# Kernel optimization log

Hardware: AMD Instinct MI355X
Metric: run time of the kernel (lower is better)

Reference implementation:

```python
import jax, jax.numpy as jnp
import numpy as np

jax.config.update("jax_enable_x64", True)  # Q16.16 int64 fixed-point arithmetic requires 64-bit ints

F = 16                 # FixedPointConfig.COMPUTE_FRAC_BITS (Q16.16)
ONE = 1 << F

B, S, D_IN, D_OUT = 2, 2048, 4096, 4096


def setup_inputs() -> dict:
    key = jax.random.key(0)
    k1, k2 = jax.random.split(key)
    x = jax.random.normal(k1, (B, S, D_IN), dtype=jnp.float32)
    weight = jax.random.normal(k2, (D_OUT, D_IN), dtype=jnp.float32)
    return {"x": x, "weight": weight}


def _to_fixed(x):
    # to_fixed_point: float -> Q16.16 int64
    return jnp.round(x * ONE).astype(jnp.int64)


def _activation_quant_fixed(xf):
    # per-token 8-bit quant/dequant, all in Q16.16 integer arithmetic
    max_vals = jnp.max(jnp.abs(xf), axis=-1, keepdims=True)
    min_val = int(1e-5 * ONE)  # == 0 at frac_bits=16 (faithful to source)
    max_vals = jnp.maximum(max_vals, min_val)
    target_max = 127 << F
    # fixed_div(target_max, max_vals, F, F, F): (a << F) // b
    scale = (target_max << F) // max_vals
    # fixed_mul(x, scale, F, F, F): (a*b) >> F  (arithmetic shift == floor-div)
    x_scaled = (xf * scale) >> F
    x_clamped = jnp.clip(x_scaled, -(128 << F), 127 << F)
    # fixed_reciprocal(scale, F, F): (1 << 2F) // scale
    scale_inv = (1 << (2 * F)) // scale
    return (x_clamped * scale_inv) >> F


def reference(x, weight):
    # --- quantize_weights() ---
    wf = _to_fixed(weight)                                   # Q16.16
    mean_abs = jnp.sum(jnp.abs(wf)) // wf.size               # fixed_mean (Q16.16 scalar)
    # fixed_div(wf, mean_abs, F, F, 0) -> integer-valued; round+clamp to {-1,0,1}
    w_ternary = jnp.clip(wf // mean_abs, -1, 1).astype(jnp.int8)

    # --- forward ---
    xq = _activation_quant_fixed(_to_fixed(x))               # [B,S,D] Q16.16 int64
    xq2 = xq.reshape(-1, D_IN)
    # Ternary GEMM replacing the per-output-feature masked-sum loop.
    # |xq| <= 128<<16 ~ 8.4e6 and K=4096 => |acc| <= 3.4e10 < 2^53, so a
    acc = jnp.dot(xq2.astype(jnp.float64), w_ternary.astype(jnp.float64).T)
    out = jnp.round(acc).astype(jnp.int64)
    out = out.astype(jnp.int32).astype(jnp.int64)            # replicate torch .to(int32) wrap
    scale_inv = (1 << (2 * F)) // mean_abs                   # fixed_reciprocal of weight_scale
    out = (out * scale_inv) >> F                             # fixed_mul dequant/rescale
    out = out.reshape(B, S, D_OUT)
    return out.astype(jnp.float32) / ONE                     # from_fixed_point
```

## Files before the change

### kernel.cpp

```cpp
#include <hip/hip_runtime.h>
#include <stdint.h>

typedef int v4i  __attribute__((ext_vector_type(4)));
typedef int v16i __attribute__((ext_vector_type(16)));

static constexpr int Mdim = 4096;
static constexpr int Ndim = 4096;
static constexpr int Kdim = 4096;

static constexpr size_t TILE_BYTES  = 128u * 4096u;
static constexpr size_t OFF_BT      = 1u << 20;
static constexpr size_t OFF_A0      = 17u << 20;
static constexpr size_t PLANE_BYTES = 16u << 20;

__device__ __forceinline__ void gload16(const void* g, void* l) {
  __builtin_amdgcn_global_load_lds(
      (const __attribute__((address_space(1))) char*)g,
      (__attribute__((address_space(3))) char*)l, 16, 0, 0);
}

__global__ void k_wsum(const float* __restrict__ w, unsigned long long* __restrict__ ws) {
  int tid = blockIdx.x * blockDim.x + threadIdx.x;
  int stride = gridDim.x * blockDim.x;
  const float4* w4 = (const float4*)w;
  const int n4 = (Ndim * Kdim) / 4;
  unsigned long long s = 0;
  for (int i = tid; i < n4; i += stride) {
    float4 v = w4[i];
    int a = (int)rintf(v.x * 65536.f);
    int b = (int)rintf(v.y * 65536.f);
    int c = (int)rintf(v.z * 65536.f);
    int d = (int)rintf(v.w * 65536.f);
    unsigned u = (unsigned)(a < 0 ? -a : a) + (unsigned)(b < 0 ? -b : b)
               + (unsigned)(c < 0 ? -c : c) + (unsigned)(d < 0 ? -d : d);
    s += u;
  }
  #pragma unroll
  for (int off = 32; off > 0; off >>= 1) s += __shfl_down(s, off, 64);
  if ((threadIdx.x & 63) == 0) atomicAdd(ws, s);
}

__global__ void k_scalars(unsigned long long* ws) {
  unsigned long long s = ws[0];
  long long mean_abs = (long long)(s >> 24);
  if (mean_abs < 1) mean_abs = 1;
  long long siw = (long long)((1ULL << 32) / (unsigned long long)mean_abs);
  ((long long*)ws)[1] = siw;
  ((long long*)ws)[2] = mean_abs;
}

__global__ void k_tern(const float* __restrict__ w, const long long* __restrict__ scal,
                       int8_t* __restrict__ bt) {
  int t = blockIdx.x * 256 + threadIdx.x;
  int mean_abs = (int)scal[2];
  int nt = t >> 15;
  int kc = (t >> 7) & 255;
  int r  = t & 127;
  int row = nt * 128 + r;
  const float4* src = (const float4*)(w + (size_t)row * Kdim + kc * 16);
  int words[4];
  #pragma unroll
  for (int j = 0; j < 4; ++j) {
    float4 v = src[j];
    float e[4] = {v.x, v.y, v.z, v.w};
    int wrd = 0;
    #pragma unroll
    for (int q = 0; q < 4; ++q) {
      int f = (int)rintf(e[q] * 65536.f);
      int tv = (f >= mean_abs ? 1 : 0) - (f < 0 ? 1 : 0);
      wrd |= (tv & 0xff) << (8 * q);
    }
    words[j] = wrd;
  }
  *(int4*)(bt + (size_t)nt * TILE_BYTES + (size_t)kc * 2048 + (size_t)r * 16) =
      make_int4(words[0], words[1], words[2], words[3]);
}

__global__ void k_actq2(const float* __restrict__ x,
                        int8_t* __restrict__ a0, int8_t* __restrict__ a1, int8_t* __restrict__ a2) {
  int m   = blockIdx.x;
  int tid = threadIdx.x;
  const float4* src = (const float4*)(x + (size_t)m * Kdim + tid * 16);
  int xf[16];
  int mx = 0;
  #pragma unroll
  for (int j = 0; j < 4; ++j) {
    float4 v = src[j];
    float e[4] = {v.x, v.y, v.z, v.w};
    #pragma unroll
    for (int q = 0; q < 4; ++q) {
      int f = (int)rintf(e[q] * 65536.f);
      xf[j * 4 + q] = f;
      int af = f < 0 ? -f : f;
      mx = af > mx ? af : mx;
    }
  }
  #pragma unroll
  for (int off = 32; off > 0; off >>= 1) {
    int o = __shfl_down(mx, off, 64);
    mx = o > mx ? o : mx;
  }
  __shared__ int red[4];
  __shared__ long long sc[2];
  if ((tid & 63) == 0) red[tid >> 6] = mx;
  __syncthreads();
  if (tid == 0) {
    int m0 = red[0];
    m0 = red[1] > m0 ? red[1] : m0;
    m0 = red[2] > m0 ? red[2] : m0;
    m0 = red[3] > m0 ? red[3] : m0;
    if (m0 < 1) m0 = 1;
    long long scale = (long long)((127ULL << 32) / (unsigned long long)m0);
    long long sinv  = (long long)((1ULL << 32) / (unsigned long long)scale);
    sc[0] = scale; sc[1] = sinv;
  }
  __syncthreads();
  long long scale = sc[0];
  long long sinv  = sc[1];

  int w0[4], w1[4], w2[4];
  #pragma unroll
  for (int j = 0; j < 4; ++j) {
    int r0 = 0, r1 = 0, r2 = 0;
    #pragma unroll
    for (int q = 0; q < 4; ++q) {
      int v  = xf[j * 4 + q];
      int xs = (int)(((long long)v * scale) >> 16);
      xs = xs < -8388608 ? -8388608 : xs;
      xs = xs > 8323072 ? 8323072 : xs;
      int xq = (int)(((long long)xs * sinv) >> 16);
      int l0 = (int)(signed char)(xq & 0xff);
      int tt = (xq - l0) >> 8;
      int l1 = (int)(signed char)(tt & 0xff);
      int l2 = (tt - l1) >> 8;
      r0 |= (l0 & 0xff) << (8 * q);
      r1 |= (l1 & 0xff) << (8 * q);
      r2 |= (l2 & 0xff) << (8 * q);
    }
    w0[j] = r0; w1[j] = r1; w2[j] = r2;
  }
  size_t idx = (size_t)(m >> 7) * TILE_BYTES + (size_t)tid * 2048 + (size_t)(m & 127) * 16;
  *(int4*)(a0 + idx) = make_int4(w0[0], w0[1], w0[2], w0[3]);
  *(int4*)(a1 + idx) = make_int4(w1[0], w1[1], w1[2], w1[3]);
  *(int4*)(a2 + idx) = make_int4(w2[0], w2[1], w2[2], w2[3]);
}

__launch_bounds__(512)
__global__ void k_gemm(const int8_t* __restrict__ a0, const int8_t* __restrict__ a1,
                       const int8_t* __restrict__ a2, const int8_t* __restrict__ bt,
                       const long long* __restrict__ scal, float* __restrict__ out) {
  __shared__ __attribute__((aligned(16))) char lds[2][5][8192];
  int bx = (blockIdx.x & 7) * 64 + (blockIdx.x >> 3);
  int mt = bx >> 4;
  int nt = bx & 15;
  int tid  = threadIdx.x;
  int lane = tid & 63;
  int w    = tid >> 6;
  int wm   = w >> 2;
  int wn   = w & 3;

  const char* planes[5];
  planes[0] = (const char*)a0 + (size_t)mt * TILE_BYTES;
  planes[1] = (const char*)a1 + (size_t)mt * TILE_BYTES;
  planes[2] = (const char*)a2 + (size_t)mt * TILE_BYTES;
  planes[3] = (const char*)bt + (size_t)(2 * nt) * TILE_BYTES;
  planes[4] = (const char*)bt + (size_t)(2 * nt + 1) * TILE_BYTES;

  v16i acc[2][2][3] = {};

  auto STAGE = [&](int buf, int kt) {
    #pragma unroll
    for (int p = 0; p < 5; ++p)
      gload16(planes[p] + (size_t)kt * 8192 + (size_t)tid * 16, &lds[buf][p][tid * 16]);
  };

  auto COMPUTE = [&](int buf) {
    #pragma unroll
    for (int ks = 0; ks < 2; ++ks) {
      const int koff = (ks * 2 + (lane >> 5)) * 2048;
      v4i afrag[2][3], bfrag[2];
      #pragma unroll
      for (int mf = 0; mf < 2; ++mf)
        #pragma unroll
        for (int p = 0; p < 3; ++p)
          afrag[mf][p] = *(const v4i*)&lds[buf][p][koff + (wm * 64 + mf * 32 + (lane & 31)) * 16];
      #pragma unroll
      for (int nj = 0; nj < 2; ++nj) {
        int col = wn * 64 + nj * 32 + (lane & 31);
        bfrag[nj] = *(const v4i*)&lds[buf][3 + (col >> 7)][koff + (col & 127) * 16];
      }
      __builtin_amdgcn_s_setprio(1);
      #pragma unroll
      for (int mf = 0; mf < 2; ++mf)
        #pragma unroll
        for (int nj = 0; nj < 2; ++nj)
          #pragma unroll
          for (int p = 0; p < 3; ++p)
            acc[mf][nj][p] = __builtin_amdgcn_mfma_i32_32x32x32_i8(
                afrag[mf][p], bfrag[nj], acc[mf][nj][p], 0, 0, 0);
      __builtin_amdgcn_s_setprio(0);
    }
  };

  const int NT = Kdim / 64;
  STAGE(0, 0);
  __syncthreads();
  for (int t = 0; t < NT; ++t) {
    int cur = t & 1;
    if (t + 1 < NT) STAGE(cur ^ 1, t + 1);
    COMPUTE(cur);
    __syncthreads();
  }

  long long siw = scal[1];
  #pragma unroll
  for (int mf = 0; mf < 2; ++mf) {
    int m0 = mt * 128 + wm * 64 + mf * 32;
    #pragma unroll
    for (int nj = 0; nj < 2; ++nj) {
      int n0 = nt * 256 + wn * 64 + nj * 32;
      #pragma unroll
      for (int rg = 0; rg < 16; ++rg) {
        unsigned u = (unsigned)acc[mf][nj][0][rg]
                   + ((unsigned)acc[mf][nj][1][rg] << 8)
                   + ((unsigned)acc[mf][nj][2][rg] << 16);
        long long v = ((long long)(int)u * siw) >> 16;
        int row = (rg & 3) + 8 * (rg >> 2) + 4 * (lane >> 5);
        int col = lane & 31;
        out[(size_t)(m0 + row) * Ndim + (n0 + col)] = (float)v * (1.f / 65536.f);
      }
    }
  }
}

extern "C" void kernel_launch(void* const* d_in, const int* in_sizes, int n_in,
                              void* d_out, int out_size, void* d_ws, size_t ws_size,
                              hipStream_t stream) {
  const float* x = (const float*)d_in[0];
  const float* w = (const float*)d_in[1];
  float* out = (float*)d_out;
  char* ws = (char*)d_ws;

  unsigned long long* scal = (unsigned long long*)ws;
  int8_t* bt = (int8_t*)(ws + OFF_BT);
  int8_t* a0 = (int8_t*)(ws + OFF_A0);
  int8_t* a1 = a0 + PLANE_BYTES;
  int8_t* a2 = a1 + PLANE_BYTES;

  hipMemsetAsync(ws, 0, 64, stream);
  k_wsum<<<1024, 256, 0, stream>>>(w, scal);
  k_scalars<<<1, 1, 0, stream>>>(scal);
  k_tern<<<4096, 256, 0, stream>>>(w, (const long long*)scal, bt);
  k_actq2<<<4096, 256, 0, stream>>>(x, a0, a1, a2);
  k_gemm<<<512, 512, 0, stream>>>(a0, a1, a2, bt, (const long long*)scal, out);
}
```

Before: 430.1 us.

## Load B fragments directly from global, split activation quant, drop scalar kernel

The GEMM no longer stages the ternary weight tiles through LDS. Each lane reads its B fragments straight from global memory, which shrinks the LDS footprint from five planes to three and cuts the staged traffic. Activation quantization is split into a coalesced row-max kernel plus a quantize kernel that writes the tiled layout with coalesced stores, and the single-thread scalar kernel is removed by recomputing mean_abs inline. The cost is that the direct global B loads must be hidden by latency tolerance within COMPUTE, and x is now read twice.

```diff
diff --git a/kernel.cpp b/kernel.cpp
--- a/kernel.cpp
+++ b/kernel.cpp
@@ -9,6 +9,7 @@
 static constexpr int Kdim = 4096;
 
 static constexpr size_t TILE_BYTES  = 128u * 4096u;
+static constexpr size_t OFF_ROWPAR  = 4096;
 static constexpr size_t OFF_BT      = 1u << 20;
 static constexpr size_t OFF_A0      = 17u << 20;
 static constexpr size_t PLANE_BYTES = 16u << 20;
@@ -40,19 +41,11 @@
   if ((threadIdx.x & 63) == 0) atomicAdd(ws, s);
 }
 
-__global__ void k_scalars(unsigned long long* ws) {
-  unsigned long long s = ws[0];
-  long long mean_abs = (long long)(s >> 24);
-  if (mean_abs < 1) mean_abs = 1;
-  long long siw = (long long)((1ULL << 32) / (unsigned long long)mean_abs);
-  ((long long*)ws)[1] = siw;
-  ((long long*)ws)[2] = mean_abs;
-}
-
-__global__ void k_tern(const float* __restrict__ w, const long long* __restrict__ scal,
+__global__ void k_tern(const float* __restrict__ w, const unsigned long long* __restrict__ ws,
                        int8_t* __restrict__ bt) {
   int t = blockIdx.x * 256 + threadIdx.x;
-  int mean_abs = (int)scal[2];
+  long long ma = (long long)(ws[0] >> 24);
+  int mean_abs = ma < 1 ? 1 : (int)ma;
   int nt = t >> 15;
   int kc = (t >> 7) & 255;
   int r  = t & 127;
@@ -76,24 +69,17 @@
       make_int4(words[0], words[1], words[2], words[3]);
 }
 
-__global__ void k_actq2(const float* __restrict__ x,
-                        int8_t* __restrict__ a0, int8_t* __restrict__ a1, int8_t* __restrict__ a2) {
-  int m   = blockIdx.x;
-  int tid = threadIdx.x;
-  const float4* src = (const float4*)(x + (size_t)m * Kdim + tid * 16);
-  int xf[16];
+__global__ void k_rowmax(const float* __restrict__ x, long long* __restrict__ rowpar) {
+  int m = blockIdx.x;
+  const float4* xr = (const float4*)(x + (size_t)m * Kdim);
   int mx = 0;
   #pragma unroll
   for (int j = 0; j < 4; ++j) {
-    float4 v = src[j];
-    float e[4] = {v.x, v.y, v.z, v.w};
-    #pragma unroll
-    for (int q = 0; q < 4; ++q) {
-      int f = (int)rintf(e[q] * 65536.f);
-      xf[j * 4 + q] = f;
-      int af = f < 0 ? -f : f;
-      mx = af > mx ? af : mx;
-    }
+    float4 v = xr[j * 256 + threadIdx.x];
+    int a = (int)rintf(v.x * 65536.f); a = a < 0 ? -a : a; mx = a > mx ? a : mx;
+    int b = (int)rintf(v.y * 65536.f); b = b < 0 ? -b : b; mx = b > mx ? b : mx;
+    int c = (int)rintf(v.z * 65536.f); c = c < 0 ? -c : c; mx = c > mx ? c : mx;
+    int d = (int)rintf(v.w * 65536.f); d = d < 0 ? -d : d; mx = d > mx ? d : mx;
   }
   #pragma unroll
   for (int off = 32; off > 0; off >>= 1) {
@@ -101,10 +87,9 @@
     mx = o > mx ? o : mx;
   }
   __shared__ int red[4];
-  __shared__ long long sc[2];
-  if ((tid & 63) == 0) red[tid >> 6] = mx;
+  if ((threadIdx.x & 63) == 0) red[threadIdx.x >> 6] = mx;
   __syncthreads();
-  if (tid == 0) {
+  if (threadIdx.x == 0) {
     int m0 = red[0];
     m0 = red[1] > m0 ? red[1] : m0;
     m0 = red[2] > m0 ? red[2] : m0;
@@ -112,20 +97,31 @@
     if (m0 < 1) m0 = 1;
     long long scale = (long long)((127ULL << 32) / (unsigned long long)m0);
     long long sinv  = (long long)((1ULL << 32) / (unsigned long long)scale);
-    sc[0] = scale; sc[1] = sinv;
-  }
-  __syncthreads();
-  long long scale = sc[0];
-  long long sinv  = sc[1];
-
+    rowpar[2 * m]     = scale;
+    rowpar[2 * m + 1] = sinv;
+  }
+}
+
+__global__ void k_actq(const float* __restrict__ x, const long long* __restrict__ rowpar,
+                       int8_t* __restrict__ a0, int8_t* __restrict__ a1, int8_t* __restrict__ a2) {
+  int t = blockIdx.x * 256 + threadIdx.x;
+  int mt = t >> 15;
+  int kc = (t >> 7) & 255;
+  int r  = t & 127;
+  int m = mt * 128 + r;
+  long long scale = rowpar[2 * m];
+  long long sinv  = rowpar[2 * m + 1];
+  const float4* src = (const float4*)(x + (size_t)m * Kdim + kc * 16);
   int w0[4], w1[4], w2[4];
   #pragma unroll
   for (int j = 0; j < 4; ++j) {
+    float4 v = src[j];
+    float e[4] = {v.x, v.y, v.z, v.w};
     int r0 = 0, r1 = 0, r2 = 0;
     #pragma unroll
     for (int q = 0; q < 4; ++q) {
-      int v  = xf[j * 4 + q];
-      int xs = (int)(((long long)v * scale) >> 16);
+      int xf = (int)rintf(e[q] * 65536.f);
+      int xs = (int)(((long long)xf * scale) >> 16);
       xs = xs < -8388608 ? -8388608 : xs;
       xs = xs > 8323072 ? 8323072 : xs;
       int xq = (int)(((long long)xs * sinv) >> 16);
@@ -139,7 +135,7 @@
     }
     w0[j] = r0; w1[j] = r1; w2[j] = r2;
   }
-  size_t idx = (size_t)(m >> 7) * TILE_BYTES + (size_t)tid * 2048 + (size_t)(m & 127) * 16;
+  size_t idx = (size_t)mt * TILE_BYTES + (size_t)kc * 2048 + (size_t)r * 16;
   *(int4*)(a0 + idx) = make_int4(w0[0], w0[1], w0[2], w0[3]);
   *(int4*)(a1 + idx) = make_int4(w1[0], w1[1], w1[2], w1[3]);
   *(int4*)(a2 + idx) = make_int4(w2[0], w2[1], w2[2], w2[3]);
@@ -148,8 +144,8 @@
 __launch_bounds__(512)
 __global__ void k_gemm(const int8_t* __restrict__ a0, const int8_t* __restrict__ a1,
                        const int8_t* __restrict__ a2, const int8_t* __restrict__ bt,
-                       const long long* __restrict__ scal, float* __restrict__ out) {
-  __shared__ __attribute__((aligned(16))) char lds[2][5][8192];
+                       const unsigned long long* __restrict__ ws, float* __restrict__ out) {
+  __shared__ __attribute__((aligned(16))) char lds[2][3][8192];
   int bx = (blockIdx.x & 7) * 64 + (blockIdx.x >> 3);
   int mt = bx >> 4;
   int nt = bx & 15;
@@ -159,36 +155,45 @@
   int wm   = w >> 2;
   int wn   = w & 3;
 
-  const char* planes[5];
-  planes[0] = (const char*)a0 + (size_t)mt * TILE_BYTES;
-  planes[1] = (const char*)a1 + (size_t)mt * TILE_BYTES;
-  planes[2] = (const char*)a2 + (size_t)mt * TILE_BYTES;
-  planes[3] = (const char*)bt + (size_t)(2 * nt) * TILE_BYTES;
-  planes[4] = (const char*)bt + (size_t)(2 * nt + 1) * TILE_BYTES;
+  const char* aplanes[3];
+  aplanes[0] = (const char*)a0 + (size_t)mt * TILE_BYTES;
+  aplanes[1] = (const char*)a1 + (size_t)mt * TILE_BYTES;
+  aplanes[2] = (const char*)a2 + (size_t)mt * TILE_BYTES;
+  const char* bbase[2];
+  #pragma unroll
+  for (int nj = 0; nj < 2; ++nj) {
+    int col = wn * 64 + nj * 32 + (lane & 31);
+    bbase[nj] = (const char*)bt + (size_t)(2 * nt + (col >> 7)) * TILE_BYTES
+              + (size_t)(col & 127) * 16 + (size_t)(lane >> 5) * 2048;
+  }
 
   v16i acc[2][2][3] = {};
 
   auto STAGE = [&](int buf, int kt) {
     #pragma unroll
-    for (int p = 0; p < 5; ++p)
-      gload16(planes[p] + (size_t)kt * 8192 + (size_t)tid * 16, &lds[buf][p][tid * 16]);
+    for (int p = 0; p < 3; ++p)
+      gload16(aplanes[p] + (size_t)kt * 8192 + (size_t)tid * 16, &lds[buf][p][tid * 16]);
   };
 
-  auto COMPUTE = [&](int buf) {
+  auto COMPUTE = [&](int buf, int kt) {
+    v4i bfrag[2][2];
+    #pragma unroll
+    for (int ks = 0; ks < 2; ++ks)
+      #pragma unroll
+      for (int nj = 0; nj < 2; ++nj)
+        bfrag[ks][nj] = *(const v4i*)(bbase[nj] + (size_t)kt * 8192 + ks * 4096);
+    v4i afrag[2][2][3];
     #pragma unroll
     for (int ks = 0; ks < 2; ++ks) {
       const int koff = (ks * 2 + (lane >> 5)) * 2048;
-      v4i afrag[2][3], bfrag[2];
       #pragma unroll
       for (int mf = 0; mf < 2; ++mf)
         #pragma unroll
         for (int p = 0; p < 3; ++p)
-          afrag[mf][p] = *(const v4i*)&lds[buf][p][koff + (wm * 64 + mf * 32 + (lane & 31)) * 16];
-      #pragma unroll
-      for (int nj = 0; nj < 2; ++nj) {
-        int col = wn * 64 + nj * 32 + (lane & 31);
-        bfrag[nj] = *(const v4i*)&lds[buf][3 + (col >> 7)][koff + (col & 127) * 16];
-      }
+          afrag[ks][mf][p] = *(const v4i*)&lds[buf][p][koff + (wm * 64 + mf * 32 + (lane & 31)) * 16];
+    }
+    #pragma unroll
+    for (int ks = 0; ks < 2; ++ks) {
       __builtin_amdgcn_s_setprio(1);
       #pragma unroll
       for (int mf = 0; mf < 2; ++mf)
@@ -197,7 +202,7 @@
           #pragma unroll
           for (int p = 0; p < 3; ++p)
             acc[mf][nj][p] = __builtin_amdgcn_mfma_i32_32x32x32_i8(
-                afrag[mf][p], bfrag[nj], acc[mf][nj][p], 0, 0, 0);
+                afrag[ks][mf][p], bfrag[ks][nj], acc[mf][nj][p], 0, 0, 0);
       __builtin_amdgcn_s_setprio(0);
     }
   };
@@ -208,11 +213,13 @@
   for (int t = 0; t < NT; ++t) {
     int cur = t & 1;
     if (t + 1 < NT) STAGE(cur ^ 1, t + 1);
-    COMPUTE(cur);
+    COMPUTE(cur, t);
     __syncthreads();
   }
 
-  long long siw = scal[1];
+  long long ma = (long long)(ws[0] >> 24);
+  if (ma < 1) ma = 1;
+  long long siw = (long long)((1ULL << 32) / (unsigned long long)ma);
   #pragma unroll
   for (int mf = 0; mf < 2; ++mf) {
     int m0 = mt * 128 + wm * 64 + mf * 32;
@@ -242,6 +249,7 @@
   char* ws = (char*)d_ws;
 
   unsigned long long* scal = (unsigned long long*)ws;
+  long long* rowpar = (long long*)(ws + OFF_ROWPAR);
   int8_t* bt = (int8_t*)(ws + OFF_BT);
   int8_t* a0 = (int8_t*)(ws + OFF_A0);
   int8_t* a1 = a0 + PLANE_BYTES;
@@ -249,8 +257,8 @@
 
   hipMemsetAsync(ws, 0, 64, stream);
   k_wsum<<<1024, 256, 0, stream>>>(w, scal);
-  k_scalars<<<1, 1, 0, stream>>>(scal);
-  k_tern<<<4096, 256, 0, stream>>>(w, (const long long*)scal, bt);
-  k_actq2<<<4096, 256, 0, stream>>>(x, a0, a1, a2);
-  k_gemm<<<512, 512, 0, stream>>>(a0, a1, a2, bt, (const long long*)scal, out);
-}
+  k_tern<<<4096, 256, 0, stream>>>(w, scal, bt);
+  k_rowmax<<<4096, 256, 0, stream>>>(x, rowpar);
+  k_actq<<<4096, 256, 0, stream>>>(x, rowpar, a0, a1, a2);
+  k_gemm<<<512, 512, 0, stream>>>(a0, a1, a2, bt, scal, out);
+}
```

After: 572.3 us. +33.1%, slower.
